# Performance work log

Measured on AMD Instinct MI355X. Metric: run time of the kernel, lower is better.

## Reference

```python
import jax, jax.numpy as jnp
import numpy as np

D_IN = 1024
D_OUT = 1024
NUM_HEADS = 16
HEAD_DIM = D_OUT // NUM_HEADS
SEQ = 2048
BATCH = 2


def setup_inputs() -> dict:
    key = jax.random.key(0)
    ks = jax.random.split(key, 6)
    s = 1.0 / np.sqrt(D_IN)
    x = jax.random.normal(ks[0], (BATCH, SEQ, D_IN), dtype=jnp.float32)
    Wq = jax.random.uniform(ks[1], (D_IN, D_OUT), jnp.float32, -s, s)
    Wk = jax.random.uniform(ks[2], (D_IN, D_OUT), jnp.float32, -s, s)
    Wv = jax.random.uniform(ks[3], (D_IN, D_OUT), jnp.float32, -s, s)
    Wo = jax.random.uniform(ks[4], (D_OUT, D_OUT), jnp.float32, -s, s)
    bo = jax.random.uniform(ks[5], (D_OUT,), jnp.float32, -s, s)
    return {"x": x, "Wq": Wq, "Wk": Wk, "Wv": Wv, "Wo": Wo, "bo": bo}


def reference(x, Wq, Wk, Wv, Wo, bo):
    b, n, _ = x.shape
    # projections, split into heads: (b, h, n, hd)
    def split_heads(t):
        return t.reshape(b, n, NUM_HEADS, HEAD_DIM).transpose(0, 2, 1, 3)
    q = split_heads(x @ Wq)
    k = split_heads(x @ Wk)
    v = split_heads(x @ Wv)
    scores = jnp.einsum("bhqd,bhkd->bhqk", q, k)
    causal = jnp.triu(jnp.ones((n, n), dtype=bool), k=1)
    scores = jnp.where(causal, -jnp.inf, scores)
    attn = jax.nn.softmax(scores / np.sqrt(HEAD_DIM), axis=-1)
    # dropout prob is 0.0 -> identity
    ctx = jnp.einsum("bhqk,bhkd->bhqd", attn, v)
    ctx = ctx.transpose(0, 2, 1, 3).reshape(b, n, D_OUT)
    return ctx @ Wo + bo
```

## Files before the change

kernel.cpp:

```cpp
#include <hip/hip_runtime.h>
#include <hip/hip_bf16.h>
#include <stdint.h>

#define D_IN   1024
#define D_OUT  1024
#define NHEAD  16
#define HDIM   64
#define SEQ    2048
#define BATCH  2
#define M_TOT  (BATCH*SEQ)

typedef __attribute__((ext_vector_type(8)))  short bfx8;
typedef __attribute__((ext_vector_type(4)))  short bfx4;
typedef __attribute__((ext_vector_type(4)))  float fx4;
typedef __attribute__((ext_vector_type(16))) float fx16;
typedef unsigned short u16;
typedef unsigned int   u32;

__device__ __forceinline__ u16 f2bf(float f) {
    u32 u = __builtin_bit_cast(u32, f);
    u32 r = (u + 0x7FFFu + ((u >> 16) & 1u)) >> 16;
    return (u16)r;
}
__device__ __forceinline__ float bf2f(u16 v) {
    u32 u = (u32)v << 16;
    return __builtin_bit_cast(float, u);
}

__device__ __forceinline__ u32 cvtpk(float lo, float hi) {
    u32 r;
    asm("v_cvt_pk_bf16_f32 %0, %1, %2" : "=v"(r) : "v"(lo), "v"(hi));
    return r;
}

__device__ __forceinline__ void gload16(const u16* g, u16* l) {
    __builtin_amdgcn_global_load_lds(
        (const __attribute__((address_space(1))) void*)g,
        (__attribute__((address_space(3))) void*)l, 16, 0, 0);
}

__global__ void k_conv_x(const float* __restrict__ x, u16* __restrict__ xb) {
    int i = blockIdx.x * 256 + threadIdx.x;
    const float4* s = reinterpret_cast<const float4*>(x);
    float4 a = s[2*i], b = s[2*i+1];
    uint4 o;
    o.x = (u32)f2bf(a.x) | ((u32)f2bf(a.y) << 16);
    o.y = (u32)f2bf(a.z) | ((u32)f2bf(a.w) << 16);
    o.z = (u32)f2bf(b.x) | ((u32)f2bf(b.y) << 16);
    o.w = (u32)f2bf(b.z) | ((u32)f2bf(b.w) << 16);
    reinterpret_cast<uint4*>(xb)[i] = o;
}

__global__ void k_conv_wt(const float* __restrict__ Wq, const float* __restrict__ Wk,
                          const float* __restrict__ Wv, const float* __restrict__ Wo,
                          u16* __restrict__ wt) {
    __shared__ float tile[32][33];
    int wsel = blockIdx.z;
    const float* W = (wsel == 0) ? Wq : (wsel == 1) ? Wk : (wsel == 2) ? Wv : Wo;
    const float scale = (wsel == 0) ? 0.125f : 1.0f;
    u16* dst = wt + (size_t)wsel * D_IN * D_OUT;
    int r0 = blockIdx.y * 32, c0 = blockIdx.x * 32;
    int tx = threadIdx.x & 31, ty = threadIdx.x >> 5;
    #pragma unroll
    for (int k = 0; k < 4; k++) {
        int i = ty + k * 8;
        tile[i][tx] = W[(size_t)(r0 + i) * D_OUT + c0 + tx];
    }
    __syncthreads();
    #pragma unroll
    for (int k = 0; k < 4; k++) {
        int i = ty + k * 8;
        dst[(size_t)(c0 + i) * D_IN + r0 + tx] = f2bf(tile[tx][i] * scale);
    }
}

template<int MODE>
__global__ __launch_bounds__(256) void k_gemm128(const u16* __restrict__ A,
                                                 const u16* __restrict__ Bt,
                                                 const float* __restrict__ bias,
                                                 u16* __restrict__ outb,
                                                 float* __restrict__ outf) {
    __shared__ u16 aL[128][32];
    __shared__ u16 bL[128][32];
    const int K = 1024;
    const int nb = blockIdx.x * 128, mb = blockIdx.y * 128;
    const int t = threadIdx.x, lane = t & 63, w = t >> 6;
    const int wr = w >> 1, wc = w & 1;
    const int li = lane & 15, lg = lane >> 4;
    const int srow = lane >> 2, schunk = (lane & 3) * 8;

    fx4 acc[4][4];
    #pragma unroll
    for (int i = 0; i < 4; i++)
        #pragma unroll
        for (int j = 0; j < 4; j++) acc[i][j] = fx4{0.f, 0.f, 0.f, 0.f};

    const u16* aBase = A  + (size_t)(mb + w * 32 + srow) * K + schunk;
    const u16* bBase = Bt + (size_t)(nb + w * 32 + srow) * K + schunk;

    for (int kb = 0; kb < K; kb += 32) {
        #pragma unroll
        for (int c = 0; c < 2; c++) {
            gload16(aBase + (size_t)c * 16 * K + kb, &aL[w * 32 + c * 16][0]);
            gload16(bBase + (size_t)c * 16 * K + kb, &bL[w * 32 + c * 16][0]);
        }
        __syncthreads();
        bfx8 af[4], bf[4];
        #pragma unroll
        for (int mi = 0; mi < 4; mi++)
            af[mi] = *reinterpret_cast<const bfx8*>(&aL[wr * 64 + mi * 16 + li][lg * 8]);
        #pragma unroll
        for (int ni = 0; ni < 4; ni++)
            bf[ni] = *reinterpret_cast<const bfx8*>(&bL[wc * 64 + ni * 16 + li][lg * 8]);
        #pragma unroll
        for (int mi = 0; mi < 4; mi++)
            #pragma unroll
            for (int ni = 0; ni < 4; ni++)
                acc[mi][ni] = __builtin_amdgcn_mfma_f32_16x16x32_bf16(af[mi], bf[ni], acc[mi][ni], 0, 0, 0);
        __syncthreads();
    }

    #pragma unroll
    for (int mi = 0; mi < 4; mi++) {
        #pragma unroll
        for (int ni = 0; ni < 4; ni++) {
            const int n = nb + wc * 64 + ni * 16 + li;
            const int m0 = mb + wr * 64 + mi * 16 + lg * 4;
            if (MODE == 0) {
                const int proj = n >> 10, h = (n >> 6) & 15, d = n & 63;
                const int b = m0 >> 11, s0 = m0 & 2047;
                if (proj == 2) {
                    u16* op = outb + (size_t)2 * M_TOT * D_OUT +
                              ((size_t)(b * NHEAD + h) * HDIM + d) * SEQ + s0;
                    bfx4 pk = {(short)f2bf(acc[mi][ni][0]), (short)f2bf(acc[mi][ni][1]),
                               (short)f2bf(acc[mi][ni][2]), (short)f2bf(acc[mi][ni][3])};
                    *reinterpret_cast<bfx4*>(op) = pk;
                } else {
                    u16* op = outb + (size_t)proj * M_TOT * D_OUT;
                    #pragma unroll
                    for (int r = 0; r < 4; r++)
                        op[((size_t)(b * NHEAD + h) * SEQ + s0 + r) * HDIM + d] =
                            f2bf(acc[mi][ni][r]);
                }
            } else {
                const float bv = bias[n];
                #pragma unroll
                for (int r = 0; r < 4; r++)
                    outf[(size_t)(m0 + r) * D_OUT + n] = acc[mi][ni][r] + bv;
            }
        }
    }
}

__global__ __launch_bounds__(128, 2) void k_attn(const u16* __restrict__ Q,
                                                 const u16* __restrict__ Kp,
                                                 const u16* __restrict__ Vt,
                                                 u16* __restrict__ ctx,
                                                 u16* __restrict__ o1,
                                                 float* __restrict__ l0,
                                                 float* __restrict__ l1) {
    __shared__ u16 kbuf[2][64][64];
    __shared__ u16 vbuf[2][64][64];

    const int g = blockIdx.x;
    int qi, part, m;
    const bool heavy = (g < 1024);
    if (heavy) {
        qi = 31 - (g >> 6);
        part = (g >> 5) & 1;
        m = g & 31;
    } else {
        int j = g - 1024;
        qi = 15 - (j >> 5);
        part = 0;
        m = j & 31;
    }
    const int bh = (m & 7) * 4 + (m >> 3);
    const int nt = qi + 1;
    int t0, t1;
    if (heavy) { int h1 = nt >> 1; t0 = part ? h1 : 0; t1 = part ? nt : h1; }
    else       { t0 = 0; t1 = nt; }
    const int ntL = t1 - t0;

    const size_t base = (size_t)bh * SEQ * HDIM;
    const int t = threadIdx.x, lane = t & 63, w = t >> 6;
    const int l31 = lane & 31, hi = lane >> 5;
    const int srow = lane >> 3;
    const int ts = (lane & 7) ^ srow;
    const int bq = bh >> 4, hh = bh & 15;
    const int swz = (l31 & 7) * 8;
    const int qwb = qi * 64 + w * 32;
    const int qg  = qwb + l31;

    auto stage = [&](int bi, int kvb) {
        #pragma unroll
        for (int i = 0; i < 4; i++) {
            const int rb = w * 32 + i * 8;
            const int rr = rb + srow;
            gload16(Kp + base + (size_t)(kvb + rr) * HDIM + ts * 8, &kbuf[bi][rb][0]);
            gload16(Vt + base + (size_t)rr * SEQ + kvb + ts * 8,    &vbuf[bi][rb][0]);
        }
    };

    bfx8 qf[4];
    #pragma unroll
    for (int dc = 0; dc < 4; dc++)
        qf[dc] = *reinterpret_cast<const bfx8*>(
            &Q[base + (size_t)qg * HDIM + dc * 16 + hi * 8]);
    fx16 cacc[2];
    #pragma unroll
    for (int dt = 0; dt < 2; dt++)
        #pragma unroll
        for (int r = 0; r < 16; r++) cacc[dt][r] = 0.f;
    float lsum = 0.f;

    stage(0, t0 * 64);

    for (int tt = 0; tt < ntL; tt++) {
        const int ti = t0 + tt;
        if (tt + 1 < ntL) {
            stage((tt + 1) & 1, (ti + 1) * 64);
            asm volatile("s_waitcnt vmcnt(8)" ::: "memory");
        } else {
            asm volatile("s_waitcnt vmcnt(0)" ::: "memory");
        }
        __builtin_amdgcn_s_barrier();
        __builtin_amdgcn_sched_barrier(0);
        const int bi = tt & 1, kvb = ti * 64;
        fx16 sc[2];
        #pragma unroll
        for (int s = 0; s < 2; s++) {
            #pragma unroll
            for (int r = 0; r < 16; r++) sc[s][r] = 0.f;
            #pragma unroll
            for (int dc = 0; dc < 4; dc++) {
                bfx8 kf = *reinterpret_cast<const bfx8*>(
                    &kbuf[bi][s * 32 + l31][(dc * 16 + hi * 8) ^ swz]);
                sc[s] = __builtin_amdgcn_mfma_f32_32x32x16_bf16(kf, qf[dc], sc[s], 0, 0, 0);
            }
        }
        if (kvb + 63 > qwb) {
            #pragma unroll
            for (int s = 0; s < 2; s++)
                #pragma unroll
                for (int r = 0; r < 16; r++) {
                    int kvg = kvb + s * 32 + (r & 3) + 8 * (r >> 2) + 4 * hi;
                    if (kvg > qg) sc[s][r] = -1e30f;
                }
        }
        float ps = 0.f;
        #pragma unroll
        for (int s = 0; s < 2; s++)
            #pragma unroll
            for (int r = 0; r < 16; r++) {
                float pv = __expf(sc[s][r]);
                sc[s][r] = pv;
                ps += pv;
            }
        lsum += ps;
        #pragma unroll
        for (int c = 0; c < 4; c++) {
            const int s = c >> 1, rb = (c & 1) * 8;
            u32 a0 = cvtpk(sc[s][rb + 0], sc[s][rb + 1]);
            u32 a1 = cvtpk(sc[s][rb + 2], sc[s][rb + 3]);
            u32 b0 = cvtpk(sc[s][rb + 4], sc[s][rb + 5]);
            u32 b1 = cvtpk(sc[s][rb + 6], sc[s][rb + 7]);
            u32 X0 = hi ? a0 : b0, X1 = hi ? a1 : b1;
            u32 Y0 = (u32)__shfl_xor((int)X0, 32);
            u32 Y1 = (u32)__shfl_xor((int)X1, 32);
            uint4 pw;
            pw.x = hi ? Y0 : a0;
            pw.y = hi ? Y1 : a1;
            pw.z = hi ? b0 : Y0;
            pw.w = hi ? b1 : Y1;
            bfx8 pf = __builtin_bit_cast(bfx8, pw);
            #pragma unroll
            for (int dt = 0; dt < 2; dt++) {
                bfx8 vf = *reinterpret_cast<const bfx8*>(
                    &vbuf[bi][dt * 32 + l31][(c * 16 + hi * 8) ^ swz]);
                cacc[dt] = __builtin_amdgcn_mfma_f32_32x32x16_bf16(pf, vf, cacc[dt], 0, 0, 0);
            }
        }
        asm volatile("s_waitcnt lgkmcnt(0)" ::: "memory");
        __builtin_amdgcn_s_barrier();
    }

    float ltot = lsum + __shfl_xor(lsum, 32);
    if (!heavy) {
        float linv = 1.0f / ltot;
        #pragma unroll
        for (int r = 0; r < 16; r++) {
            const int qpat = (r & 3) + 8 * (r >> 2) + 4 * hi;
            float rl = __shfl(linv, qpat);
            const int q = qwb + qpat;
            #pragma unroll
            for (int dt = 0; dt < 2; dt++)
                ctx[((size_t)(bq * SEQ + q)) * D_OUT + hh * HDIM + dt * 32 + l31] =
                    f2bf(cacc[dt][r] * rl);
        }
    } else {
        const int qi16 = qi - 16;
        const int lidx = ((qi16 * 32 + bh) * 64) + w * 32 + l31;
        if (hi == 0) { (part ? l1 : l0)[lidx] = ltot; }
        #pragma unroll
        for (int r = 0; r < 16; r++) {
            const int qpat = (r & 3) + 8 * (r >> 2) + 4 * hi;
            const int q = qwb + qpat;
            #pragma unroll
            for (int dt = 0; dt < 2; dt++) {
                const int d = dt * 32 + l31;
                u16 val = f2bf(cacc[dt][r]);
                if (part == 0)
                    ctx[((size_t)(bq * SEQ + q)) * D_OUT + hh * HDIM + d] = val;
                else
                    o1[(((size_t)(qi16 * 32 + bh) * 64) + w * 32 + qpat) * 64 + d] = val;
            }
        }
    }
}

__global__ void k_comb(u16* __restrict__ ctx, const u16* __restrict__ o1,
                       const float* __restrict__ l0, const float* __restrict__ l1) {
    int i = blockIdx.x * 256 + threadIdx.x;
    const int d    = (i & 7) * 8;
    const int qrow = (i >> 3) & 63;
    const int bi_  = i >> 9;
    const int bh   = bi_ & 31, qi16 = bi_ >> 5;
    const int bq = bh >> 4, hh = bh & 15;
    const int token = bq * SEQ + (16 + qi16) * 64 + qrow;
    const size_t cidx = (size_t)token * D_OUT + hh * HDIM + d;
    const size_t oidx = ((size_t)(bi_ * 64 + qrow)) * 64 + d;
    const float linv = 1.0f / (l0[bi_ * 64 + qrow] + l1[bi_ * 64 + qrow]);
    bfx8 a = *reinterpret_cast<const bfx8*>(&ctx[cidx]);
    bfx8 b = *reinterpret_cast<const bfx8*>(&o1[oidx]);
    bfx8 o;
    #pragma unroll
    for (int j = 0; j < 8; j++)
        o[j] = (short)f2bf((bf2f((u16)a[j]) + bf2f((u16)b[j])) * linv);
    *reinterpret_cast<bfx8*>(&ctx[cidx]) = o;
}

extern "C" void kernel_launch(void* const* d_in, const int* in_sizes, int n_in,
                              void* d_out, int out_size, void* d_ws, size_t ws_size,
                              hipStream_t stream) {
    const float* x  = (const float*)d_in[0];
    const float* Wq = (const float*)d_in[1];
    const float* Wk = (const float*)d_in[2];
    const float* Wv = (const float*)d_in[3];
    const float* Wo = (const float*)d_in[4];
    const float* bo = (const float*)d_in[5];
    float* out = (float*)d_out;

    char* ws = (char*)d_ws;
    u16* xb   = (u16*)(ws);
    u16* wt   = (u16*)(ws + (8u << 20));
    u16* qkvb = (u16*)(ws + (16u << 20));
    u16* ctxb = (u16*)(ws + (40u << 20));

    u16*   o1p = (u16*)(ws);
    float* l0p = (float*)(ws + (4u << 20));
    float* l1p = (float*)(ws + (4u << 20) + (128u << 10));

    const u16* Qb  = qkvb;
    const u16* Kb  = qkvb + (size_t)M_TOT * D_OUT;
    const u16* Vtb = qkvb + (size_t)2 * M_TOT * D_OUT;

    k_conv_x <<<2048, 256, 0, stream>>>(x, xb);
    k_conv_wt<<<dim3(32, 32, 4), 256, 0, stream>>>(Wq, Wk, Wv, Wo, wt);
    k_gemm128<0><<<dim3(24, 32), 256, 0, stream>>>(xb, wt, nullptr, qkvb, nullptr);
    k_attn   <<<dim3(1536), 128, 0, stream>>>(Qb, Kb, Vtb, ctxb, o1p, l0p, l1p);
    k_comb   <<<1024, 256, 0, stream>>>(ctxb, o1p, l0p, l1p);
    k_gemm128<1><<<dim3(8, 32), 256, 0, stream>>>(
        ctxb, wt + (size_t)3 * D_IN * D_OUT, bo, nullptr, out);
}
```

Measured before the change: 116.1 us.

## Enlarge attention blocks to 256 query rows with shared KV staging

The attention kernel now uses 512-thread blocks (8 waves) that each cover 256 query rows instead of 64, so each K/V tile staged in shared memory is reused by four times as many waves and global K/V traffic drops. Heavy/light work assignment moves to a constant lookup table over 12 query-tile groups, with split-KV halves for the upper tiles, and the combine kernel indexing is updated to match. Waves whose queries lie entirely above the current KV tile skip the compute, which leaves those waves idle at barriers inside the block. Fewer, larger blocks (384) reduce scheduling granularity and occupancy flexibility in exchange.

```diff
diff --git a/kernel.cpp b/kernel.cpp
--- a/kernel.cpp
+++ b/kernel.cpp
@@ -152,7 +152,7 @@
     }
 }
 
-__global__ __launch_bounds__(128, 2) void k_attn(const u16* __restrict__ Q,
+__global__ __launch_bounds__(512, 2) void k_attn(const u16* __restrict__ Q,
                                                  const u16* __restrict__ Kp,
                                                  const u16* __restrict__ Vt,
                                                  u16* __restrict__ ctx,
@@ -162,21 +162,15 @@
     __shared__ u16 kbuf[2][64][64];
     __shared__ u16 vbuf[2][64][64];
 
-    const int g = blockIdx.x;
-    int qi, part, m;
-    const bool heavy = (g < 1024);
-    if (heavy) {
-        qi = 31 - (g >> 6);
-        part = (g >> 5) & 1;
-        m = g & 31;
-    } else {
-        int j = g - 1024;
-        qi = 15 - (j >> 5);
-        part = 0;
-        m = j & 31;
-    }
+    static const __constant__ signed char QT[12]   = {7,7,6,6,5,5,4,4,3,2,1,0};
+    static const __constant__ signed char PART[12] = {0,1,0,1,0,1,0,1,0,0,0,0};
+
+    const int g  = blockIdx.x;
+    const int m  = g & 31, pp = g >> 5;
     const int bh = (m & 7) * 4 + (m >> 3);
-    const int nt = qi + 1;
+    const int qt = QT[pp], part = PART[pp];
+    const bool heavy = (qt >= 4);
+    const int nt = 4 * qt + 4;
     int t0, t1;
     if (heavy) { int h1 = nt >> 1; t0 = part ? h1 : 0; t1 = part ? nt : h1; }
     else       { t0 = 0; t1 = nt; }
@@ -189,17 +183,15 @@
     const int ts = (lane & 7) ^ srow;
     const int bq = bh >> 4, hh = bh & 15;
     const int swz = (l31 & 7) * 8;
-    const int qwb = qi * 64 + w * 32;
+    const int qwb = qt * 256 + w * 32;
     const int qg  = qwb + l31;
 
     auto stage = [&](int bi, int kvb) {
-        #pragma unroll
-        for (int i = 0; i < 4; i++) {
-            const int rb = w * 32 + i * 8;
-            const int rr = rb + srow;
-            gload16(Kp + base + (size_t)(kvb + rr) * HDIM + ts * 8, &kbuf[bi][rb][0]);
-            gload16(Vt + base + (size_t)rr * SEQ + kvb + ts * 8,    &vbuf[bi][rb][0]);
-        }
+        const int rb = w * 8;
+        gload16(Kp + base + (size_t)(kvb + rb + srow) * HDIM + ts * 8,
+                &kbuf[bi][rb][0]);
+        gload16(Vt + base + (size_t)(rb + srow) * SEQ + kvb + ts * 8,
+                &vbuf[bi][rb][0]);
     };
 
     bfx8 qf[4];
@@ -217,68 +209,70 @@
     stage(0, t0 * 64);
 
     for (int tt = 0; tt < ntL; tt++) {
-        const int ti = t0 + tt;
+        const int ti = t0 + tt, kvb = ti * 64;
         if (tt + 1 < ntL) {
             stage((tt + 1) & 1, (ti + 1) * 64);
-            asm volatile("s_waitcnt vmcnt(8)" ::: "memory");
+            asm volatile("s_waitcnt vmcnt(2)" ::: "memory");
         } else {
             asm volatile("s_waitcnt vmcnt(0)" ::: "memory");
         }
         __builtin_amdgcn_s_barrier();
         __builtin_amdgcn_sched_barrier(0);
-        const int bi = tt & 1, kvb = ti * 64;
-        fx16 sc[2];
-        #pragma unroll
-        for (int s = 0; s < 2; s++) {
-            #pragma unroll
-            for (int r = 0; r < 16; r++) sc[s][r] = 0.f;
-            #pragma unroll
-            for (int dc = 0; dc < 4; dc++) {
-                bfx8 kf = *reinterpret_cast<const bfx8*>(
-                    &kbuf[bi][s * 32 + l31][(dc * 16 + hi * 8) ^ swz]);
-                sc[s] = __builtin_amdgcn_mfma_f32_32x32x16_bf16(kf, qf[dc], sc[s], 0, 0, 0);
-            }
-        }
-        if (kvb + 63 > qwb) {
+        const int bi = tt & 1;
+        if (kvb <= qwb + 31) {
+            fx16 sc[2];
+            #pragma unroll
+            for (int s = 0; s < 2; s++) {
+                #pragma unroll
+                for (int r = 0; r < 16; r++) sc[s][r] = 0.f;
+                #pragma unroll
+                for (int dc = 0; dc < 4; dc++) {
+                    bfx8 kf = *reinterpret_cast<const bfx8*>(
+                        &kbuf[bi][s * 32 + l31][(dc * 16 + hi * 8) ^ swz]);
+                    sc[s] = __builtin_amdgcn_mfma_f32_32x32x16_bf16(kf, qf[dc], sc[s], 0, 0, 0);
+                }
+            }
+            if (kvb + 63 > qwb) {
+                #pragma unroll
+                for (int s = 0; s < 2; s++)
+                    #pragma unroll
+                    for (int r = 0; r < 16; r++) {
+                        int kvg = kvb + s * 32 + (r & 3) + 8 * (r >> 2) + 4 * hi;
+                        if (kvg > qg) sc[s][r] = -1e30f;
+                    }
+            }
+            float ps = 0.f;
             #pragma unroll
             for (int s = 0; s < 2; s++)
                 #pragma unroll
                 for (int r = 0; r < 16; r++) {
-                    int kvg = kvb + s * 32 + (r & 3) + 8 * (r >> 2) + 4 * hi;
-                    if (kvg > qg) sc[s][r] = -1e30f;
+                    float pv = __expf(sc[s][r]);
+                    sc[s][r] = pv;
+                    ps += pv;
                 }
-        }
-        float ps = 0.f;
-        #pragma unroll
-        for (int s = 0; s < 2; s++)
-            #pragma unroll
-            for (int r = 0; r < 16; r++) {
-                float pv = __expf(sc[s][r]);
-                sc[s][r] = pv;
-                ps += pv;
-            }
-        lsum += ps;
-        #pragma unroll
-        for (int c = 0; c < 4; c++) {
-            const int s = c >> 1, rb = (c & 1) * 8;
-            u32 a0 = cvtpk(sc[s][rb + 0], sc[s][rb + 1]);
-            u32 a1 = cvtpk(sc[s][rb + 2], sc[s][rb + 3]);
-            u32 b0 = cvtpk(sc[s][rb + 4], sc[s][rb + 5]);
-            u32 b1 = cvtpk(sc[s][rb + 6], sc[s][rb + 7]);
-            u32 X0 = hi ? a0 : b0, X1 = hi ? a1 : b1;
-            u32 Y0 = (u32)__shfl_xor((int)X0, 32);
-            u32 Y1 = (u32)__shfl_xor((int)X1, 32);
-            uint4 pw;
-            pw.x = hi ? Y0 : a0;
-            pw.y = hi ? Y1 : a1;
-            pw.z = hi ? b0 : Y0;
-            pw.w = hi ? b1 : Y1;
-            bfx8 pf = __builtin_bit_cast(bfx8, pw);
-            #pragma unroll
-            for (int dt = 0; dt < 2; dt++) {
-                bfx8 vf = *reinterpret_cast<const bfx8*>(
-                    &vbuf[bi][dt * 32 + l31][(c * 16 + hi * 8) ^ swz]);
-                cacc[dt] = __builtin_amdgcn_mfma_f32_32x32x16_bf16(pf, vf, cacc[dt], 0, 0, 0);
+            lsum += ps;
+            #pragma unroll
+            for (int c = 0; c < 4; c++) {
+                const int s = c >> 1, rb_ = (c & 1) * 8;
+                u32 a0 = cvtpk(sc[s][rb_ + 0], sc[s][rb_ + 1]);
+                u32 a1 = cvtpk(sc[s][rb_ + 2], sc[s][rb_ + 3]);
+                u32 b0 = cvtpk(sc[s][rb_ + 4], sc[s][rb_ + 5]);
+                u32 b1 = cvtpk(sc[s][rb_ + 6], sc[s][rb_ + 7]);
+                u32 X0 = hi ? a0 : b0, X1 = hi ? a1 : b1;
+                u32 Y0 = (u32)__shfl_xor((int)X0, 32);
+                u32 Y1 = (u32)__shfl_xor((int)X1, 32);
+                uint4 pw;
+                pw.x = hi ? Y0 : a0;
+                pw.y = hi ? Y1 : a1;
+                pw.z = hi ? b0 : Y0;
+                pw.w = hi ? b1 : Y1;
+                bfx8 pf = __builtin_bit_cast(bfx8, pw);
+                #pragma unroll
+                for (int dt = 0; dt < 2; dt++) {
+                    bfx8 vf = *reinterpret_cast<const bfx8*>(
+                        &vbuf[bi][dt * 32 + l31][(c * 16 + hi * 8) ^ swz]);
+                    cacc[dt] = __builtin_amdgcn_mfma_f32_32x32x16_bf16(pf, vf, cacc[dt], 0, 0, 0);
+                }
             }
         }
         asm volatile("s_waitcnt lgkmcnt(0)" ::: "memory");
@@ -299,9 +293,9 @@
                     f2bf(cacc[dt][r] * rl);
         }
     } else {
-        const int qi16 = qi - 16;
-        const int lidx = ((qi16 * 32 + bh) * 64) + w * 32 + l31;
-        if (hi == 0) { (part ? l1 : l0)[lidx] = ltot; }
+        const int qt4 = qt - 4;
+        const int rbase = (qt4 * 32 + bh) * 256 + w * 32;
+        if (hi == 0) { (part ? l1 : l0)[rbase + l31] = ltot; }
         #pragma unroll
         for (int r = 0; r < 16; r++) {
             const int qpat = (r & 3) + 8 * (r >> 2) + 4 * hi;
@@ -313,7 +307,7 @@
                 if (part == 0)
                     ctx[((size_t)(bq * SEQ + q)) * D_OUT + hh * HDIM + d] = val;
                 else
-                    o1[(((size_t)(qi16 * 32 + bh) * 64) + w * 32 + qpat) * 64 + d] = val;
+                    o1[((size_t)(rbase + qpat)) * 64 + d] = val;
             }
         }
     }
@@ -323,14 +317,15 @@
                        const float* __restrict__ l0, const float* __restrict__ l1) {
     int i = blockIdx.x * 256 + threadIdx.x;
     const int d    = (i & 7) * 8;
-    const int qrow = (i >> 3) & 63;
-    const int bi_  = i >> 9;
-    const int bh   = bi_ & 31, qi16 = bi_ >> 5;
+    const int qrow = (i >> 3) & 255;
+    const int bi_  = i >> 11;
+    const int bh   = bi_ & 31, qt4 = bi_ >> 5;
     const int bq = bh >> 4, hh = bh & 15;
-    const int token = bq * SEQ + (16 + qi16) * 64 + qrow;
+    const int token = bq * SEQ + (4 + qt4) * 256 + qrow;
     const size_t cidx = (size_t)token * D_OUT + hh * HDIM + d;
-    const size_t oidx = ((size_t)(bi_ * 64 + qrow)) * 64 + d;
-    const float linv = 1.0f / (l0[bi_ * 64 + qrow] + l1[bi_ * 64 + qrow]);
+    const int ridx = bi_ * 256 + qrow;
+    const size_t oidx = (size_t)ridx * 64 + d;
+    const float linv = 1.0f / (l0[ridx] + l1[ridx]);
     bfx8 a = *reinterpret_cast<const bfx8*>(&ctx[cidx]);
     bfx8 b = *reinterpret_cast<const bfx8*>(&o1[oidx]);
     bfx8 o;
@@ -368,7 +363,7 @@
     k_conv_x <<<2048, 256, 0, stream>>>(x, xb);
     k_conv_wt<<<dim3(32, 32, 4), 256, 0, stream>>>(Wq, Wk, Wv, Wo, wt);
     k_gemm128<0><<<dim3(24, 32), 256, 0, stream>>>(xb, wt, nullptr, qkvb, nullptr);
-    k_attn   <<<dim3(1536), 128, 0, stream>>>(Qb, Kb, Vtb, ctxb, o1p, l0p, l1p);
+    k_attn   <<<dim3(384), 512, 0, stream>>>(Qb, Kb, Vtb, ctxb, o1p, l0p, l1p);
     k_comb   <<<1024, 256, 0, stream>>>(ctxb, o1p, l0p, l1p);
     k_gemm128<1><<<dim3(8, 32), 256, 0, stream>>>(
         ctxb, wt + (size_t)3 * D_IN * D_OUT, bo, nullptr, out);
```

After: 115.6 us. Within noise of the previous version (-0.4%).
